# Optimization experiments

Hardware: AMD Instinct MI355X
Metric: run time of the kernel (lower is better)

The kernel has to match this reference:

```python
import jax, jax.numpy as jnp
import numpy as np

N_NODES = 50000


def _sage_conv(x, src, dst, W_l, b_l, W_r, n_nodes):
    # mean-aggregate neighbor (source) features onto targets
    msg = x[src]                                   # [E, d_in] gather
    agg = jax.ops.segment_sum(msg, dst, num_segments=n_nodes)   # [N, d_in]
    deg = jax.ops.segment_sum(jnp.ones((src.shape[0],), x.dtype), dst,
                              num_segments=n_nodes)
    agg = agg / jnp.clip(deg, 1.0, None)[:, None]  # mean with deg>=1 clamp (PyG)
    # out = lin_l(agg) + lin_r(x)   (bias lives in lin_l)
    return agg @ W_l.T + b_l + x @ W_r.T


def setup_inputs() -> dict:
    key = jax.random.key(0)
    ks = jax.random.split(key, 8)
    d_in, d_hid, d_out = 128, 256, 128
    n_edges = 800000
    x = jax.random.normal(ks[0], (N_NODES, d_in), dtype=jnp.float32)
    edge_index = jax.random.randint(ks[1], (2, n_edges), 0, N_NODES, dtype=jnp.int32)
    def glorot(k, shape):
        lim = float(np.sqrt(6.0 / (shape[0] + shape[1])))
        return jax.random.uniform(k, shape, jnp.float32, -lim, lim)
    return {
        "x": x,
        "edge_index": edge_index,
        "W1l": glorot(ks[2], (d_hid, d_in)),
        "b1": jnp.zeros((d_hid,), jnp.float32),
        "W1r": glorot(ks[3], (d_hid, d_in)),
        "W2l": glorot(ks[4], (d_out, d_hid)),
        "b2": jnp.zeros((d_out,), jnp.float32),
        "W2r": glorot(ks[5], (d_out, d_hid)),
    }


def reference(x, edge_index, W1l, b1, W1r, W2l, b2, W2r):
    src, dst = edge_index[0], edge_index[1]
    h = jax.nn.relu(_sage_conv(x, src, dst, W1l, b1, W1r, N_NODES))
    out = _sage_conv(h, src, dst, W2l, b2, W2r, N_NODES)
    return out
```

## Files before the change

### kernel.cpp

```cpp
#include <hip/hip_runtime.h>
#include <hip/hip_bf16.h>

#define NN 50000
#define NN_PAD 50176
#define NE 800000
#define NB 196
#define CAP 6144
#define EPB 4096

typedef __attribute__((ext_vector_type(8))) short short8;
typedef __attribute__((ext_vector_type(4))) float f32x4;
typedef __attribute__((ext_vector_type(2))) float f32x2;
typedef __attribute__((ext_vector_type(4))) unsigned int u32x4;
typedef __attribute__((ext_vector_type(2))) unsigned int u32x2;

__device__ __forceinline__ unsigned short f2bf(float f) {
    union { float f; unsigned u; } v; v.f = f;
    unsigned u = v.u;
    return (unsigned short)((u + 0x7fffu + ((u >> 16) & 1u)) >> 16);
}
__device__ __forceinline__ float bfu_lo(unsigned u) {
    union { unsigned u; float f; } v; v.u = u << 16; return v.f;
}
__device__ __forceinline__ float bfu_hi(unsigned u) {
    union { unsigned u; float f; } v; v.u = u & 0xffff0000u; return v.f;
}
__device__ __forceinline__ void acc_fp8(float* acc, uint2 q) {
    f32x2 a0 = __builtin_amdgcn_cvt_pk_f32_fp8(q.x, false);
    f32x2 a1 = __builtin_amdgcn_cvt_pk_f32_fp8(q.x, true);
    f32x2 a2 = __builtin_amdgcn_cvt_pk_f32_fp8(q.y, false);
    f32x2 a3 = __builtin_amdgcn_cvt_pk_f32_fp8(q.y, true);
    acc[0] += a0.x; acc[1] += a0.y; acc[2] += a1.x; acc[3] += a1.y;
    acc[4] += a2.x; acc[5] += a2.y; acc[6] += a3.x; acc[7] += a3.y;
}


__global__ void k_setup_part(const float* __restrict__ W1l, const float* __restrict__ W1r,
                             const float* __restrict__ W2l, const float* __restrict__ W2r,
                             unsigned short* __restrict__ W1pk, unsigned short* __restrict__ W2pk,
                             const float* __restrict__ x, unsigned short* __restrict__ xbf,
                             unsigned char* __restrict__ x_f8,
                             const int* __restrict__ src, const int* __restrict__ dst,
                             int* __restrict__ gcursor, unsigned* __restrict__ pairs) {
    int blk = blockIdx.x, t = threadIdx.x;
    if (blk < NB) {
        __shared__ int cnt[256];
        __shared__ int cur[256];
        __shared__ int base[256];
        cnt[t] = 0; cur[t] = 0;
        __syncthreads();
        int e0 = blk * EPB;
        int eend = min(e0 + EPB, NE);
        for (int e = e0 + t; e < eend; e += 256)
            atomicAdd(&cnt[dst[e] >> 8], 1);
        __syncthreads();
        if (t < NB && cnt[t] > 0) base[t] = t * CAP + atomicAdd(&gcursor[t], cnt[t]);
        __syncthreads();
        for (int e = e0 + t; e < eend; e += 256) {
            int s = src[e], d = dst[e];
            int bk = d >> 8;
            int pos = base[bk] + atomicAdd(&cur[bk], 1);
            if (pos < (bk + 1) * CAP) pairs[pos] = ((unsigned)s << 8) | (unsigned)(d & 255);
        }
    } else if (blk < 260) {
        int tid = (blk - 196) * 256 + t;
        int table = tid >> 13;
        int r = tid & 8191;
        int lane = r & 63, ni = (r >> 6) & 3, ks = (r >> 8) & 7, g = r >> 11;
        int lm = lane & 15, lq = lane >> 4;
        int o = g * 64 + ni * 16 + lm;
        int k = ks * 32 + lq * 8;
        unsigned short v[8];
        if (table == 0) {
            if (k < 128) {
#pragma unroll
                for (int j = 0; j < 8; ++j) v[j] = f2bf(W1l[o * 128 + k + j]);
            } else {
#pragma unroll
                for (int j = 0; j < 8; ++j) v[j] = f2bf(W1r[o * 128 + k - 128 + j]);
            }
            *(uint4*)(W1pk + (size_t)r * 8) = *(const uint4*)v;
        } else {
            if (o < 128) {
#pragma unroll
                for (int j = 0; j < 8; ++j) v[j] = f2bf(W2l[o * 256 + k + j]);
            } else {
#pragma unroll
                for (int j = 0; j < 8; ++j) v[j] = f2bf(W2r[(o - 128) * 256 + k + j]);
            }
            *(uint4*)(W2pk + (size_t)r * 8) = *(const uint4*)v;
        }
    } else {
        int gid = (blk - 260) * 256 + t;
        int n = gid >> 5, c = gid & 31;
        f32x4 v = __builtin_nontemporal_load((const f32x4*)x + (size_t)n * 32 + c);
        unsigned short o[4];
        o[0] = f2bf(v[0]); o[1] = f2bf(v[1]); o[2] = f2bf(v[2]); o[3] = f2bf(v[3]);
        *(u32x2*)(xbf + (size_t)n * 128 + c * 4) = *(const u32x2*)o;
        unsigned p = (unsigned)__builtin_amdgcn_cvt_pk_fp8_f32(v[0], v[1], 0, false);
        p = (unsigned)__builtin_amdgcn_cvt_pk_fp8_f32(v[2], v[3], (int)p, true);
        *(unsigned*)(x_f8 + (size_t)n * 128 + c * 4) = p;
    }
}

__global__ void k_build(const int* __restrict__ gcursor, const unsigned* __restrict__ pairs,
                        unsigned* __restrict__ meta, unsigned short* __restrict__ esrc) {
    __shared__ int buf[256];
    __shared__ int ldeg[256];
    __shared__ int cur[256];
    __shared__ int sh_base, sh_cnt;
    __shared__ unsigned short lsrc[CAP];
    __shared__ unsigned lp[CAP];
    int b = blockIdx.x, t = threadIdx.x;
    int c = (t < NB) ? min(gcursor[t], CAP) : 0;
    buf[t] = c;
    __syncthreads();
#pragma unroll
    for (int o = 1; o < 256; o <<= 1) {
        int add = (t >= o) ? buf[t - o] : 0;
        __syncthreads();
        buf[t] += add;
        __syncthreads();
    }
    if (t == b) { sh_cnt = c; sh_base = buf[b] - c; }
    ldeg[t] = 0;
    __syncthreads();
    int cnt = sh_cnt, base = sh_base;
    for (int e = t; e < cnt; e += 256) {
        unsigned p = pairs[(size_t)b * CAP + e];
        lp[e] = p;
        atomicAdd(&ldeg[p & 255u], 1);
    }
    __syncthreads();
    int v = ldeg[t];
    buf[t] = v;
    __syncthreads();
#pragma unroll
    for (int o = 1; o < 256; o <<= 1) {
        int add = (t >= o) ? buf[t - o] : 0;
        __syncthreads();
        buf[t] += add;
        __syncthreads();
    }
    int lst = buf[t] - v;
    cur[t] = lst;
    int node = b * 256 + t;
    meta[node] = (node < NN) ? ((unsigned)(base + lst) | ((unsigned)v << 20)) : 0u;
    __syncthreads();
    for (int e = t; e < cnt; e += 256) {
        unsigned p = lp[e];
        int pos = atomicAdd(&cur[p & 255u], 1);
        lsrc[pos] = (unsigned short)(p >> 8);
    }
    __syncthreads();
    for (int e = t; e < cnt; e += 256) esrc[base + e] = lsrc[e];
}

__global__ __launch_bounds__(256, 2) void k_gemm12(
        const unsigned short* __restrict__ xbf, const uint2* __restrict__ xf8,
        const unsigned* __restrict__ meta, const unsigned short* __restrict__ esrc,
        const unsigned short* __restrict__ W1pk, const unsigned short* __restrict__ W2pk,
        const float* __restrict__ b1, const float* __restrict__ b2,
        unsigned char* __restrict__ y2f8, unsigned short* __restrict__ Sbf) {
    __shared__ unsigned short T[16384];
    int t = threadIdx.x, blk = blockIdx.x;
    int wave = t >> 6, lane = t & 63;
    int lm = lane & 15, lq = lane >> 4;
    int pbase = lm * 4 + lq;

    short8 w[8][4];
    {
        const unsigned short* wb = W1pk + (size_t)wave * 16384;
#pragma unroll
        for (int ks = 0; ks < 8; ++ks)
#pragma unroll
            for (int ni = 0; ni < 4; ++ni)
                w[ks][ni] = *(const short8*)(wb + ((size_t)((ks * 4 + ni) * 64 + lane)) * 8);
    }

    {
        int cc = t & 15, rb = t >> 4;
        int ks2 = cc >> 2, lq2 = cc & 3;
        for (int mi2 = 0; mi2 < 4; ++mi2) {
            int n = blk * 64 + mi2 * 16 + rb;
            unsigned mt = meta[n];
            int st = (int)(mt & 0xFFFFFu), dg = (int)(mt >> 20);
            float acc[8] = {0.f, 0.f, 0.f, 0.f, 0.f, 0.f, 0.f, 0.f};
            int i = 0;
            for (; i + 4 <= dg; i += 4) {
                int s0 = esrc[st + i],     s1 = esrc[st + i + 1];
                int s2 = esrc[st + i + 2], s3 = esrc[st + i + 3];
                uint2 q0 = xf8[(size_t)s0 * 16 + cc];
                uint2 q1 = xf8[(size_t)s1 * 16 + cc];
                uint2 q2 = xf8[(size_t)s2 * 16 + cc];
                uint2 q3 = xf8[(size_t)s3 * 16 + cc];
                acc_fp8(acc, q0); acc_fp8(acc, q1); acc_fp8(acc, q2); acc_fp8(acc, q3);
            }
            for (; i < dg; ++i) {
                int s = esrc[st + i];
                acc_fp8(acc, xf8[(size_t)s * 16 + cc]);
            }
            float invd = 1.0f / (float)max(dg, 1);
            unsigned short o[8];
#pragma unroll
            for (int j = 0; j < 8; ++j) o[j] = f2bf(acc[j] * invd);
            *(u32x4*)(T + ((size_t)((ks2 * 4 + mi2) * 64 + rb + 16 * lq2)) * 8) = *(const u32x4*)o;
        }
    }
    {
        int r = t >> 2, d0 = (t & 3) * 32;
        int mi2 = r >> 4, lmr = r & 15;
        const unsigned short* xr = xbf + (size_t)(blk * 64 + r) * 128 + d0;
#pragma unroll
        for (int q = 0; q < 4; ++q) {
            u32x4 v = __builtin_nontemporal_load((const u32x4*)xr + q);
            int d = d0 + q * 8;
            int ks2 = 4 + (d >> 5), lq2 = (d >> 3) & 3;
            *(u32x4*)(T + ((size_t)((ks2 * 4 + mi2) * 64 + lmr + 16 * lq2)) * 8) = v;
        }
    }
    __syncthreads();

    f32x4 acc1[4][4];
#pragma unroll
    for (int mi = 0; mi < 4; ++mi)
#pragma unroll
        for (int ni = 0; ni < 4; ++ni) acc1[mi][ni] = (f32x4){0.f, 0.f, 0.f, 0.f};
#pragma unroll
    for (int ks = 0; ks < 8; ++ks) {
        short8 a[4];
#pragma unroll
        for (int mi = 0; mi < 4; ++mi)
            a[mi] = *(const short8*)(T + ((size_t)((ks * 4 + mi) * 64 + lane)) * 8);
#pragma unroll
        for (int mi = 0; mi < 4; ++mi)
#pragma unroll
            for (int ni = 0; ni < 4; ++ni)
                acc1[mi][ni] = __builtin_amdgcn_mfma_f32_16x16x32_bf16(a[mi], w[ks][ni], acc1[mi][ni], 0, 0, 0);
    }

    {
        const unsigned short* wb = W2pk + (size_t)wave * 16384;
#pragma unroll
        for (int ks = 0; ks < 8; ++ks)
#pragma unroll
            for (int ni = 0; ni < 4; ++ni)
                w[ks][ni] = *(const short8*)(wb + ((size_t)((ks * 4 + ni) * 64 + lane)) * 8);
    }
    __syncthreads();

#pragma unroll
    for (int ni = 0; ni < 4; ++ni) {
        int col = wave * 64 + ni * 16 + lm;
        float bv = b1[col];
        int ks = col >> 5;
        int la = (col & 31) >> 3, j = col & 7;
#pragma unroll
        for (int mi = 0; mi < 4; ++mi)
#pragma unroll
            for (int r = 0; r < 4; ++r) {
                float v = fmaxf(acc1[mi][ni][r] + bv, 0.0f);
                T[((size_t)((ks * 4 + mi) * 64 + (lq * 4 + r) * 4 + la)) * 8 + j] = f2bf(v);
            }
    }
    __syncthreads();

    f32x4 acc2[4][4];
#pragma unroll
    for (int mi = 0; mi < 4; ++mi)
#pragma unroll
        for (int ni = 0; ni < 4; ++ni) acc2[mi][ni] = (f32x4){0.f, 0.f, 0.f, 0.f};
#pragma unroll
    for (int ks = 0; ks < 8; ++ks) {
        short8 a[4];
#pragma unroll
        for (int mi = 0; mi < 4; ++mi)
            a[mi] = *(const short8*)(T + ((size_t)((ks * 4 + mi) * 64 + pbase)) * 8);
#pragma unroll
        for (int mi = 0; mi < 4; ++mi)
#pragma unroll
            for (int ni = 0; ni < 4; ++ni)
                acc2[mi][ni] = __builtin_amdgcn_mfma_f32_16x16x32_bf16(a[mi], w[ks][ni], acc2[mi][ni], 0, 0, 0);
    }
    __syncthreads();

    {
        unsigned char* T8 = (unsigned char*)T;
        unsigned short* T16 = (unsigned short*)T + 4096;
        if (wave < 2) {
#pragma unroll
            for (int ni = 0; ni < 4; ++ni) {
                int col = wave * 64 + ni * 16 + lm;
#pragma unroll
                for (int mi = 0; mi < 4; ++mi)
#pragma unroll
                    for (int r = 0; r < 4; ++r) {
                        int rl = mi * 16 + lq * 4 + r;
                        float v = acc2[mi][ni][r];
                        unsigned p = (unsigned)__builtin_amdgcn_cvt_pk_fp8_f32(v, v, 0, false);
                        T8[rl * 128 + col] = (unsigned char)(p & 0xff);
                    }
            }
        } else {
#pragma unroll
            for (int ni = 0; ni < 4; ++ni) {
                int col = (wave - 2) * 64 + ni * 16 + lm;
                float bv = b2[col];
#pragma unroll
                for (int mi = 0; mi < 4; ++mi)
#pragma unroll
                    for (int r = 0; r < 4; ++r) {
                        int rl = mi * 16 + lq * 4 + r;
                        T16[rl * 128 + col] = f2bf(acc2[mi][ni][r] + bv);
                    }
            }
        }
    }
    __syncthreads();

    {
        const uint4* Ty = (const uint4*)T;
        uint4* gy = (uint4*)(y2f8 + (size_t)blk * 64 * 128);
        gy[t] = Ty[t];
        gy[t + 256] = Ty[t + 256];
        const u32x4* Ts = (const u32x4*)((const char*)T + 8192);
        u32x4* gs = (u32x4*)(Sbf + (size_t)blk * 64 * 128);
#pragma unroll
        for (int i = 0; i < 4; ++i)
            __builtin_nontemporal_store(Ts[t + i * 256], &gs[t + i * 256]);
    }
}

__global__ void k_agg_out(const uint2* __restrict__ yf8, const unsigned short* __restrict__ Sbf,
                          const unsigned* __restrict__ meta,
                          const unsigned short* __restrict__ esrc,
                          float* __restrict__ out) {
    int gid = blockIdx.x * blockDim.x + threadIdx.x;
    int n = gid >> 4, c = gid & 15;
    unsigned mt = meta[n];
    int st = (int)(mt & 0xFFFFFu), dg = (int)(mt >> 20);
    float acc[8] = {0.f, 0.f, 0.f, 0.f, 0.f, 0.f, 0.f, 0.f};
    int i = 0;
    for (; i + 4 <= dg; i += 4) {
        int s0 = esrc[st + i],     s1 = esrc[st + i + 1];
        int s2 = esrc[st + i + 2], s3 = esrc[st + i + 3];
        uint2 q0 = yf8[(size_t)s0 * 16 + c];
        uint2 q1 = yf8[(size_t)s1 * 16 + c];
        uint2 q2 = yf8[(size_t)s2 * 16 + c];
        uint2 q3 = yf8[(size_t)s3 * 16 + c];
        acc_fp8(acc, q0); acc_fp8(acc, q1); acc_fp8(acc, q2); acc_fp8(acc, q3);
    }
    for (; i < dg; ++i) {
        int s = esrc[st + i];
        acc_fp8(acc, yf8[(size_t)s * 16 + c]);
    }
    float invd = 1.0f / (float)max(dg, 1);
    u32x4 sv = __builtin_nontemporal_load((const u32x4*)Sbf + (size_t)n * 16 + c);
    f32x4 o0, o1;
    o0[0] = bfu_lo(sv[0]) + acc[0] * invd; o0[1] = bfu_hi(sv[0]) + acc[1] * invd;
    o0[2] = bfu_lo(sv[1]) + acc[2] * invd; o0[3] = bfu_hi(sv[1]) + acc[3] * invd;
    o1[0] = bfu_lo(sv[2]) + acc[4] * invd; o1[1] = bfu_hi(sv[2]) + acc[5] * invd;
    o1[2] = bfu_lo(sv[3]) + acc[6] * invd; o1[3] = bfu_hi(sv[3]) + acc[7] * invd;
    f32x4* op = (f32x4*)(out + (size_t)n * 128 + c * 8);
    __builtin_nontemporal_store(o0, op);
    __builtin_nontemporal_store(o1, op + 1);
}

extern "C" void kernel_launch(void* const* d_in, const int* in_sizes, int n_in,
                              void* d_out, int out_size, void* d_ws, size_t ws_size,
                              hipStream_t stream) {
    const float* x   = (const float*)d_in[0];
    const int*   ei  = (const int*)d_in[1];
    const int*   src = ei;
    const int*   dst = ei + NE;
    const float* W1l = (const float*)d_in[2];
    const float* b1  = (const float*)d_in[3];
    const float* W1r = (const float*)d_in[4];
    const float* W2l = (const float*)d_in[5];
    const float* b2  = (const float*)d_in[6];
    const float* W2r = (const float*)d_in[7];
    float* out = (float*)d_out;

    char* ws = (char*)d_ws;
    unsigned* meta        = (unsigned*)(ws + 0);
    int* gcursor          = (int*)(ws + 204800);
    unsigned short* esrc  = (unsigned short*)(ws + 208896);
    unsigned* pairs       = (unsigned*)(ws + 2097152);
    unsigned short* Sbf   = (unsigned short*)(ws + 8388608);
    unsigned char* x_f8   = (unsigned char*)(ws + 25165824);
    unsigned char* y2f8   = (unsigned char*)(ws + 33554432);
    unsigned short* xbf   = (unsigned short*)(ws + 41943040);
    unsigned short* W1pk  = (unsigned short*)(ws + 56623104);
    unsigned short* W2pk  = (unsigned short*)(ws + 56754176);

    hipMemsetAsync(gcursor, 0, 1024, stream);
    k_setup_part<<<6510, 256, 0, stream>>>(W1l, W1r, W2l, W2r, W1pk, W2pk,
                                           x, xbf, x_f8, src, dst, gcursor, pairs);
    k_build<<<NB, 256, 0, stream>>>(gcursor, pairs, meta, esrc);
    k_gemm12<<<NN_PAD / 64, 256, 0, stream>>>(xbf, (const uint2*)x_f8, meta, esrc,
                                              W1pk, W2pk, b1, b2, y2f8, Sbf);
    k_agg_out<<<NN * 16 / 256, 256, 0, stream>>>((const uint2*)y2f8, Sbf,
                                                 meta, esrc, out);
}
```

Baseline: 204.2 us.

## Split layer-1 aggregation into separate kernel writing MFMA-packed A tiles

Moves the layer-1 neighbor mean aggregation out of the GEMM kernel into a standalone high-occupancy gather kernel that writes bf16 results straight into a pre-swizzled MFMA operand layout. The setup kernel also writes x's bf16 copy into that packed layout, so the GEMM reads A fragments directly from global memory with no LDS staging or barriers. It also widens k_build to 1024 threads and unrolls the gathers by 8. The cost is an extra launch and a global round trip for the packed A matrix, in exchange for removing the latency-bound gather from the register-heavy GEMM with its limited occupancy.

```diff
diff --git a/kernel.cpp b/kernel.cpp
--- a/kernel.cpp
+++ b/kernel.cpp
@@ -38,7 +38,7 @@
 __global__ void k_setup_part(const float* __restrict__ W1l, const float* __restrict__ W1r,
                              const float* __restrict__ W2l, const float* __restrict__ W2r,
                              unsigned short* __restrict__ W1pk, unsigned short* __restrict__ W2pk,
-                             const float* __restrict__ x, unsigned short* __restrict__ xbf,
+                             const float* __restrict__ x, unsigned short* __restrict__ Apk,
                              unsigned char* __restrict__ x_f8,
                              const int* __restrict__ src, const int* __restrict__ dst,
                              int* __restrict__ gcursor, unsigned* __restrict__ pairs) {
@@ -96,7 +96,11 @@
         f32x4 v = __builtin_nontemporal_load((const f32x4*)x + (size_t)n * 32 + c);
         unsigned short o[4];
         o[0] = f2bf(v[0]); o[1] = f2bf(v[1]); o[2] = f2bf(v[2]); o[3] = f2bf(v[3]);
-        *(u32x2*)(xbf + (size_t)n * 128 + c * 4) = *(const u32x2*)o;
+        int k = 128 + c * 4;
+        int ks = k >> 5, lq = (k >> 3) & 3, j0 = k & 7;
+        int tile = n >> 6, r = n & 63, mi = r >> 4, lm = r & 15;
+        *(u32x2*)(Apk + (size_t)tile * 16384 +
+                  ((size_t)((ks * 4 + mi) * 64 + lm + 16 * lq)) * 8 + j0) = *(const u32x2*)o;
         unsigned p = (unsigned)__builtin_amdgcn_cvt_pk_fp8_f32(v[0], v[1], 0, false);
         p = (unsigned)__builtin_amdgcn_cvt_pk_fp8_f32(v[2], v[3], (int)p, true);
         *(unsigned*)(x_f8 + (size_t)n * 128 + c * 4) = p;
@@ -113,52 +117,92 @@
     __shared__ unsigned lp[CAP];
     int b = blockIdx.x, t = threadIdx.x;
     int c = (t < NB) ? min(gcursor[t], CAP) : 0;
-    buf[t] = c;
+    if (t < 256) buf[t] = c;
     __syncthreads();
 #pragma unroll
     for (int o = 1; o < 256; o <<= 1) {
-        int add = (t >= o) ? buf[t - o] : 0;
-        __syncthreads();
-        buf[t] += add;
+        int add = (t < 256 && t >= o) ? buf[t - o] : 0;
+        __syncthreads();
+        if (t < 256) buf[t] += add;
         __syncthreads();
     }
     if (t == b) { sh_cnt = c; sh_base = buf[b] - c; }
-    ldeg[t] = 0;
+    if (t < 256) ldeg[t] = 0;
     __syncthreads();
     int cnt = sh_cnt, base = sh_base;
-    for (int e = t; e < cnt; e += 256) {
+    for (int e = t; e < cnt; e += 1024) {
         unsigned p = pairs[(size_t)b * CAP + e];
         lp[e] = p;
         atomicAdd(&ldeg[p & 255u], 1);
     }
     __syncthreads();
-    int v = ldeg[t];
-    buf[t] = v;
+    int v = (t < 256) ? ldeg[t] : 0;
+    if (t < 256) buf[t] = v;
     __syncthreads();
 #pragma unroll
     for (int o = 1; o < 256; o <<= 1) {
-        int add = (t >= o) ? buf[t - o] : 0;
-        __syncthreads();
-        buf[t] += add;
-        __syncthreads();
-    }
-    int lst = buf[t] - v;
-    cur[t] = lst;
-    int node = b * 256 + t;
-    meta[node] = (node < NN) ? ((unsigned)(base + lst) | ((unsigned)v << 20)) : 0u;
-    __syncthreads();
-    for (int e = t; e < cnt; e += 256) {
+        int add = (t < 256 && t >= o) ? buf[t - o] : 0;
+        __syncthreads();
+        if (t < 256) buf[t] += add;
+        __syncthreads();
+    }
+    if (t < 256) {
+        int lst = buf[t] - v;
+        cur[t] = lst;
+        int node = b * 256 + t;
+        meta[node] = (node < NN) ? ((unsigned)(base + lst) | ((unsigned)v << 20)) : 0u;
+    }
+    __syncthreads();
+    for (int e = t; e < cnt; e += 1024) {
         unsigned p = lp[e];
         int pos = atomicAdd(&cur[p & 255u], 1);
         lsrc[pos] = (unsigned short)(p >> 8);
     }
     __syncthreads();
-    for (int e = t; e < cnt; e += 256) esrc[base + e] = lsrc[e];
+    for (int e = t; e < cnt; e += 1024) esrc[base + e] = lsrc[e];
+}
+
+__global__ void k_agg1(const uint2* __restrict__ xf8, const unsigned* __restrict__ meta,
+                       const unsigned short* __restrict__ esrc,
+                       unsigned short* __restrict__ Apk) {
+    int gid = blockIdx.x * blockDim.x + threadIdx.x;
+    int n = gid >> 4, c = gid & 15;
+    unsigned mt = meta[n];
+    int st = (int)(mt & 0xFFFFFu), dg = (int)(mt >> 20);
+    float acc[8] = {0.f, 0.f, 0.f, 0.f, 0.f, 0.f, 0.f, 0.f};
+    int i = 0;
+    for (; i + 8 <= dg; i += 8) {
+        int s0 = esrc[st + i],     s1 = esrc[st + i + 1];
+        int s2 = esrc[st + i + 2], s3 = esrc[st + i + 3];
+        int s4 = esrc[st + i + 4], s5 = esrc[st + i + 5];
+        int s6 = esrc[st + i + 6], s7 = esrc[st + i + 7];
+        uint2 q0 = xf8[(size_t)s0 * 16 + c];
+        uint2 q1 = xf8[(size_t)s1 * 16 + c];
+        uint2 q2 = xf8[(size_t)s2 * 16 + c];
+        uint2 q3 = xf8[(size_t)s3 * 16 + c];
+        uint2 q4 = xf8[(size_t)s4 * 16 + c];
+        uint2 q5 = xf8[(size_t)s5 * 16 + c];
+        uint2 q6 = xf8[(size_t)s6 * 16 + c];
+        uint2 q7 = xf8[(size_t)s7 * 16 + c];
+        acc_fp8(acc, q0); acc_fp8(acc, q1); acc_fp8(acc, q2); acc_fp8(acc, q3);
+        acc_fp8(acc, q4); acc_fp8(acc, q5); acc_fp8(acc, q6); acc_fp8(acc, q7);
+    }
+    for (; i < dg; ++i) {
+        int s = esrc[st + i];
+        acc_fp8(acc, xf8[(size_t)s * 16 + c]);
+    }
+    float invd = 1.0f / (float)max(dg, 1);
+    unsigned short o[8];
+#pragma unroll
+    for (int j = 0; j < 8; ++j) o[j] = f2bf(acc[j] * invd);
+    int ks = c >> 2, lq = c & 3;
+    int tile = n >> 6, r = n & 63, mi = r >> 4, lm = r & 15;
+    *(u32x4*)(Apk + (size_t)tile * 16384 +
+              ((size_t)((ks * 4 + mi) * 64 + lm + 16 * lq)) * 8) = *(const u32x4*)o;
 }
 
 __global__ __launch_bounds__(256, 2) void k_gemm12(
-        const unsigned short* __restrict__ xbf, const uint2* __restrict__ xf8,
-        const unsigned* __restrict__ meta, const unsigned short* __restrict__ esrc,
+        const unsigned short* __restrict__ Apk,
         const unsigned short* __restrict__ W1pk, const unsigned short* __restrict__ W2pk,
         const float* __restrict__ b1, const float* __restrict__ b2,
         unsigned char* __restrict__ y2f8, unsigned short* __restrict__ Sbf) {
@@ -178,49 +222,7 @@
                 w[ks][ni] = *(const short8*)(wb + ((size_t)((ks * 4 + ni) * 64 + lane)) * 8);
     }
 
-    {
-        int cc = t & 15, rb = t >> 4;
-        int ks2 = cc >> 2, lq2 = cc & 3;
-        for (int mi2 = 0; mi2 < 4; ++mi2) {
-            int n = blk * 64 + mi2 * 16 + rb;
-            unsigned mt = meta[n];
-            int st = (int)(mt & 0xFFFFFu), dg = (int)(mt >> 20);
-            float acc[8] = {0.f, 0.f, 0.f, 0.f, 0.f, 0.f, 0.f, 0.f};
-            int i = 0;
-            for (; i + 4 <= dg; i += 4) {
-                int s0 = esrc[st + i],     s1 = esrc[st + i + 1];
-                int s2 = esrc[st + i + 2], s3 = esrc[st + i + 3];
-                uint2 q0 = xf8[(size_t)s0 * 16 + cc];
-                uint2 q1 = xf8[(size_t)s1 * 16 + cc];
-                uint2 q2 = xf8[(size_t)s2 * 16 + cc];
-                uint2 q3 = xf8[(size_t)s3 * 16 + cc];
-                acc_fp8(acc, q0); acc_fp8(acc, q1); acc_fp8(acc, q2); acc_fp8(acc, q3);
-            }
-            for (; i < dg; ++i) {
-                int s = esrc[st + i];
-                acc_fp8(acc, xf8[(size_t)s * 16 + cc]);
-            }
-            float invd = 1.0f / (float)max(dg, 1);
-            unsigned short o[8];
-#pragma unroll
-            for (int j = 0; j < 8; ++j) o[j] = f2bf(acc[j] * invd);
-            *(u32x4*)(T + ((size_t)((ks2 * 4 + mi2) * 64 + rb + 16 * lq2)) * 8) = *(const u32x4*)o;
-        }
-    }
-    {
-        int r = t >> 2, d0 = (t & 3) * 32;
-        int mi2 = r >> 4, lmr = r & 15;
-        const unsigned short* xr = xbf + (size_t)(blk * 64 + r) * 128 + d0;
-#pragma unroll
-        for (int q = 0; q < 4; ++q) {
-            u32x4 v = __builtin_nontemporal_load((const u32x4*)xr + q);
-            int d = d0 + q * 8;
-            int ks2 = 4 + (d >> 5), lq2 = (d >> 3) & 3;
-            *(u32x4*)(T + ((size_t)((ks2 * 4 + mi2) * 64 + lmr + 16 * lq2)) * 8) = v;
-        }
-    }
-    __syncthreads();
-
+    const unsigned short* apk = Apk + (size_t)blk * 16384;
     f32x4 acc1[4][4];
 #pragma unroll
     for (int mi = 0; mi < 4; ++mi)
@@ -231,7 +233,7 @@
         short8 a[4];
 #pragma unroll
         for (int mi = 0; mi < 4; ++mi)
-            a[mi] = *(const short8*)(T + ((size_t)((ks * 4 + mi) * 64 + lane)) * 8);
+            a[mi] = *(const short8*)(apk + ((size_t)((ks * 4 + mi) * 64 + lane)) * 8);
 #pragma unroll
         for (int mi = 0; mi < 4; ++mi)
 #pragma unroll
@@ -247,7 +249,6 @@
             for (int ni = 0; ni < 4; ++ni)
                 w[ks][ni] = *(const short8*)(wb + ((size_t)((ks * 4 + ni) * 64 + lane)) * 8);
     }
-    __syncthreads();
 
 #pragma unroll
     for (int ni = 0; ni < 4; ++ni) {
@@ -341,14 +342,21 @@
     int st = (int)(mt & 0xFFFFFu), dg = (int)(mt >> 20);
     float acc[8] = {0.f, 0.f, 0.f, 0.f, 0.f, 0.f, 0.f, 0.f};
     int i = 0;
-    for (; i + 4 <= dg; i += 4) {
+    for (; i + 8 <= dg; i += 8) {
         int s0 = esrc[st + i],     s1 = esrc[st + i + 1];
         int s2 = esrc[st + i + 2], s3 = esrc[st + i + 3];
+        int s4 = esrc[st + i + 4], s5 = esrc[st + i + 5];
+        int s6 = esrc[st + i + 6], s7 = esrc[st + i + 7];
         uint2 q0 = yf8[(size_t)s0 * 16 + c];
         uint2 q1 = yf8[(size_t)s1 * 16 + c];
         uint2 q2 = yf8[(size_t)s2 * 16 + c];
         uint2 q3 = yf8[(size_t)s3 * 16 + c];
+        uint2 q4 = yf8[(size_t)s4 * 16 + c];
+        uint2 q5 = yf8[(size_t)s5 * 16 + c];
+        uint2 q6 = yf8[(size_t)s6 * 16 + c];
+        uint2 q7 = yf8[(size_t)s7 * 16 + c];
         acc_fp8(acc, q0); acc_fp8(acc, q1); acc_fp8(acc, q2); acc_fp8(acc, q3);
+        acc_fp8(acc, q4); acc_fp8(acc, q5); acc_fp8(acc, q6); acc_fp8(acc, q7);
     }
     for (; i < dg; ++i) {
         int s = esrc[st + i];
@@ -383,22 +391,22 @@
 
     char* ws = (char*)d_ws;
     unsigned* meta        = (unsigned*)(ws + 0);
-    int* gcursor          = (int*)(ws + 204800);
-    unsigned short* esrc  = (unsigned short*)(ws + 208896);
-    unsigned* pairs       = (unsigned*)(ws + 2097152);
-    unsigned short* Sbf   = (unsigned short*)(ws + 8388608);
-    unsigned char* x_f8   = (unsigned char*)(ws + 25165824);
-    unsigned char* y2f8   = (unsigned char*)(ws + 33554432);
-    unsigned short* xbf   = (unsigned short*)(ws + 41943040);
-    unsigned short* W1pk  = (unsigned short*)(ws + 56623104);
-    unsigned short* W2pk  = (unsigned short*)(ws + 56754176);
+    int* gcursor          = (int*)(ws + 401408);
+    unsigned short* esrc  = (unsigned short*)(ws + 409600);
+    unsigned* pairs       = (unsigned*)(ws + 4194304);
+    unsigned short* Sbf   = (unsigned short*)(ws + 9437184);
+    unsigned char* x_f8   = (unsigned char*)(ws + 22282240);
+    unsigned char* y2f8   = (unsigned char*)(ws + 28704768);
+    unsigned short* Apk   = (unsigned short*)(ws + 35651584);
+    unsigned short* W1pk  = (unsigned short*)(ws + 61341696);
+    unsigned short* W2pk  = (unsigned short*)(ws + 61472768);
 
     hipMemsetAsync(gcursor, 0, 1024, stream);
     k_setup_part<<<6510, 256, 0, stream>>>(W1l, W1r, W2l, W2r, W1pk, W2pk,
-                                           x, xbf, x_f8, src, dst, gcursor, pairs);
-    k_build<<<NB, 256, 0, stream>>>(gcursor, pairs, meta, esrc);
-    k_gemm12<<<NN_PAD / 64, 256, 0, stream>>>(xbf, (const uint2*)x_f8, meta, esrc,
-                                              W1pk, W2pk, b1, b2, y2f8, Sbf);
+                                           x, Apk, x_f8, src, dst, gcursor, pairs);
+    k_build<<<NB, 1024, 0, stream>>>(gcursor, pairs, meta, esrc);
+    k_agg1<<<NN * 16 / 256, 256, 0, stream>>>((const uint2*)x_f8, meta, esrc, Apk);
+    k_gemm12<<<NN_PAD / 64, 256, 0, stream>>>(Apk, W1pk, W2pk, b1, b2, y2f8, Sbf);
     k_agg_out<<<NN * 16 / 256, 256, 0, stream>>>((const uint2*)y2f8, Sbf,
                                                  meta, esrc, out);
 }
```

Measured after the change: 185.8 us. -9.0%, faster.
